# Kernel tuning notes

Hardware: AMD Instinct MI355X
Metric: run time of the kernel (lower is better)

Reference implementation:

```python
import jax, jax.numpy as jnp
import numpy as np

B, S, HID = 2, 2048, 1024
H, HKV, D = 16, 8, 128
G = H // HKV
EPS = 1e-6
ROPE_BASE = 1e6


def _rms_norm(x, w):
    # per-last-dim RMSNorm in fp32, matching QwenRMSNorm
    x32 = x.astype(jnp.float32)
    var = jnp.mean(x32 * x32, axis=-1, keepdims=True)
    return w * (x32 * jax.lax.rsqrt(var + EPS)).astype(x.dtype)


def _rotate_half(x):
    half = x.shape[-1] // 2
    return jnp.concatenate([-x[..., half:], x[..., :half]], axis=-1)


def setup_inputs() -> dict:
    key = jax.random.key(0)
    ks = jax.random.split(key, 6)
    return {
        "hidden_states": jax.random.normal(ks[0], (B, S, HID), dtype=jnp.float32),
        "position_ids": jnp.arange(S, dtype=jnp.int32),
        "Wq": jax.random.normal(ks[1], (HID, H * D), dtype=jnp.float32) * 0.02,
        "Wk": jax.random.normal(ks[2], (HID, HKV * D), dtype=jnp.float32) * 0.02,
        "Wv": jax.random.normal(ks[3], (HID, HKV * D), dtype=jnp.float32) * 0.02,
        "Wo": jax.random.normal(ks[4], (H * D, HID), dtype=jnp.float32) * 0.02,
        "q_norm_w": jnp.ones((D,), dtype=jnp.float32),
        "k_norm_w": jnp.ones((D,), dtype=jnp.float32),
    }


def reference(hidden_states, position_ids, Wq, Wk, Wv, Wo, q_norm_w, k_norm_w):
    b, s, _ = hidden_states.shape
    # projections
    q = (hidden_states @ Wq).reshape(b, s, H, D)
    k = (hidden_states @ Wk).reshape(b, s, HKV, D)
    v = (hidden_states @ Wv).reshape(b, s, HKV, D)
    # QK RMSNorm (per head_dim), then [B, heads, S, D]
    q = _rms_norm(q, q_norm_w).transpose(0, 2, 1, 3)
    k = _rms_norm(k, k_norm_w).transpose(0, 2, 1, 3)
    v = v.transpose(0, 2, 1, 3)
    # RoPE
    inv_freq = 1.0 / (ROPE_BASE ** (jnp.arange(0, D, 2, dtype=jnp.float32) / D))
    freqs = position_ids.astype(jnp.float32)[:, None] * inv_freq[None, :]  # [S, D/2]
    emb = jnp.concatenate([freqs, freqs], axis=-1)  # [S, D]
    cos = jnp.cos(emb)[None, None, :, :].astype(q.dtype)
    sin = jnp.sin(emb)[None, None, :, :].astype(q.dtype)
    q = q * cos + _rotate_half(q) * sin
    k = k * cos + _rotate_half(k) * sin
    # GQA attention without materializing repeated K/V:
    # q heads h = kh*G + g  <->  repeat_interleave(G, dim=1) of kv heads
    qg = q.reshape(b, HKV, G, s, D)
    scale = 1.0 / jnp.sqrt(jnp.asarray(D, dtype=q.dtype))
    scores = jnp.einsum('bhgqd,bhkd->bhgqk', qg, k) * scale  # [B,HKV,G,S,S]
    causal = jnp.tril(jnp.ones((s, s), dtype=bool))
    scores = jnp.where(causal[None, None, None, :, :], scores, jnp.finfo(scores.dtype).min)
    probs = jax.nn.softmax(scores, axis=-1)
    attn = jnp.einsum('bhgqk,bhkd->bhgqd', probs, v)  # [B,HKV,G,S,D]
    attn = attn.reshape(b, H, s, D).transpose(0, 2, 1, 3).reshape(b, s, H * D)
    out = attn @ Wo
    return out, k, v
```

## Files before the change

kernel.cpp:

```cpp
#include <hip/hip_runtime.h>

#define B_ 2
#define S_ 2048
#define HID_ 1024
#define H_ 16
#define HKV_ 8
#define D_ 128

typedef unsigned short u16;
typedef __attribute__((ext_vector_type(8))) short short8;
typedef __attribute__((ext_vector_type(4))) float f32x4;
typedef __attribute__((ext_vector_type(16))) float f32x16;
typedef __attribute__((ext_vector_type(2))) unsigned short u16x2;
typedef __attribute__((ext_vector_type(4))) unsigned short u16x4;
typedef const __attribute__((address_space(1))) void gvoid;
typedef __attribute__((address_space(3))) void svoid;

__device__ __forceinline__ u16 f2b(float f) {
  union { float f; unsigned u; } v; v.f = f;
  unsigned r = v.u + 0x7FFFu + ((v.u >> 16) & 1u);
  return (u16)(r >> 16);
}
__device__ __forceinline__ float b2f(u16 x) {
  union { unsigned u; float f; } v; v.u = ((unsigned)x) << 16; return v.f;
}

__device__ __forceinline__ float exp2_fast(float x) {
  float r; asm("v_exp_f32 %0, %1" : "=v"(r) : "v"(x)); return r;
}
__device__ __forceinline__ unsigned cvtpk_bf16(float lo, float hi) {
  unsigned r; asm("v_cvt_pk_bf16_f32 %0, %1, %2" : "=v"(r) : "v"(lo), "v"(hi)); return r;
}
__device__ __forceinline__ void vm_drain() {
  asm volatile("s_waitcnt vmcnt(0)" ::: "memory");
  __builtin_amdgcn_sched_barrier(0);
}

__global__ __launch_bounds__(256) void conv_bf16_kernel(const float* __restrict__ X,
                                                        u16* __restrict__ Y, int n4) {
  int i = blockIdx.x * 256 + threadIdx.x;
  if (i < n4) {
    const float4 v = ((const float4*)X)[i];
    u16x4 o = { f2b(v.x), f2b(v.y), f2b(v.z), f2b(v.w) };
    ((u16x4*)Y)[i] = o;
  }
}

template <bool PERM>
__global__ __launch_bounds__(256) void transpose_bf16_kernel(const float* __restrict__ W,
                                                             u16* __restrict__ Wt,
                                                             int K, int N) {
  __shared__ float t[32][33];
  const int nb = N >> 5;
  const int bx = blockIdx.x % nb;
  const int by = blockIdx.x / nb;
  const int tx = threadIdx.x & 31, ty = threadIdx.x >> 5;
#pragma unroll
  for (int i = 0; i < 32; i += 8)
    t[ty + i][tx] = W[(size_t)(by * 32 + ty + i) * N + bx * 32 + tx];
  __syncthreads();
#pragma unroll
  for (int i = 0; i < 32; i += 8) {
    int n = bx * 32 + ty + i;
    int nn;
    if (PERM) {
      int head = n >> 7, d = n & 127;
      int p = (d & 15) | (((d >> 6) & 1) << 4) | (((d >> 4) & 1) << 5) | (((d >> 5) & 1) << 6);
      nn = head * 128 + p;
    } else {
      nn = n;
    }
    Wt[(size_t)nn * K + by * 32 + tx] = f2b(t[tx][ty + i]);
  }
}

__global__ __launch_bounds__(256) void rope_table_kernel(const int* __restrict__ pid,
                                                         float* __restrict__ ct,
                                                         float* __restrict__ st) {
  int i = blockIdx.x * 256 + threadIdx.x;
  if (i >= 64 * S_) return;
  int f = i >> 11, s = i & 2047;
  double inv = exp2(-(double)f * (19.931568569324174 / 64.0));
  double ang = (double)pid[s] * inv;
  ct[i] = (float)cos(ang);
  st[i] = (float)sin(ang);
}

template <int M, int N, int K, int BM>
__global__ __launch_bounds__(256) void gemm_bt(const u16* __restrict__ A,
                                               const u16* __restrict__ Bt,
                                               float* __restrict__ C) {
  __shared__ u16 As[BM * 64];
  __shared__ u16 Bs[128 * 64];
  const int tid = threadIdx.x;
  const int w = tid >> 6;
  const int l = tid & 63;
  const int l15 = l & 15, lg = l >> 4;
  const int nbx = N / 128;
  const int bx = blockIdx.x % nbx, by = blockIdx.x / nbx;
  const int row0 = by * BM, col0 = bx * 128;
  const int wr = w >> 1, wc = w & 1;
  constexpr int MR = BM / 32;

  f32x4 acc[MR][4];
#pragma unroll
  for (int m = 0; m < MR; ++m)
#pragma unroll
    for (int n = 0; n < 4; ++n) acc[m][n] = (f32x4){0.f, 0.f, 0.f, 0.f};

  for (int k0 = 0; k0 < K; k0 += 64) {
    __syncthreads();
#pragma unroll
    for (int i = 0; i < BM / 32; ++i) {
      int c = i * 256 + tid;
      int r = c >> 3, cc = c & 7;
      int cs = cc ^ ((r ^ (r >> 3)) & 7);
      const u16* sa = A + (size_t)(row0 + r) * K + k0 + cs * 8;
      __builtin_amdgcn_global_load_lds((gvoid*)sa, (svoid*)(As + (i * 256 + w * 64) * 8), 16, 0, 0);
    }
#pragma unroll
    for (int i = 0; i < 4; ++i) {
      int c = i * 256 + tid;
      int r = c >> 3, cc = c & 7;
      int cs = cc ^ ((r ^ (r >> 3)) & 7);
      const u16* sb = Bt + (size_t)(col0 + r) * K + k0 + cs * 8;
      __builtin_amdgcn_global_load_lds((gvoid*)sb, (svoid*)(Bs + (i * 256 + w * 64) * 8), 16, 0, 0);
    }
    vm_drain();
    __syncthreads();
#pragma unroll
    for (int kk = 0; kk < 2; ++kk) {
      short8 af[MR], bf[4];
#pragma unroll
      for (int m = 0; m < MR; ++m) {
        const int row = wr * (BM / 2) + m * 16 + l15;
        af[m] = *(const short8*)((const char*)As + row * 128 +
                                 (((kk * 4 + lg) ^ ((row ^ (row >> 3)) & 7)) << 4));
      }
#pragma unroll
      for (int n = 0; n < 4; ++n) {
        const int row = wc * 64 + n * 16 + l15;
        bf[n] = *(const short8*)((const char*)Bs + row * 128 +
                                 (((kk * 4 + lg) ^ ((row ^ (row >> 3)) & 7)) << 4));
      }
#pragma unroll
      for (int m = 0; m < MR; ++m)
#pragma unroll
        for (int n = 0; n < 4; ++n)
          acc[m][n] = __builtin_amdgcn_mfma_f32_16x16x32_bf16(af[m], bf[n], acc[m][n], 0, 0, 0);
    }
  }
#pragma unroll
  for (int m = 0; m < MR; ++m)
#pragma unroll
    for (int n = 0; n < 4; ++n) {
      float* cp = C + (size_t)(row0 + wr * (BM / 2) + m * 16 + lg * 4) * N + col0 + wc * 64 + n * 16 + l15;
#pragma unroll
      for (int r = 0; r < 4; ++r) cp[(size_t)r * N] = acc[m][n][r];
    }
}

__global__ __launch_bounds__(256) void gemm_qkv_fused(const u16* __restrict__ A,
                                                      const u16* __restrict__ Bt,
                                                      const float* __restrict__ qnw,
                                                      const float* __restrict__ knw,
                                                      const float* __restrict__ ct_t,
                                                      const float* __restrict__ st_t,
                                                      u16* __restrict__ Qbb,
                                                      u16* __restrict__ Kbb,
                                                      float* __restrict__ kout,
                                                      float* __restrict__ vout,
                                                      u16* __restrict__ VTb) {
  constexpr int K = 1024;
  __shared__ u16 As[64 * 64];
  __shared__ u16 Bs[128 * 64];
  __shared__ float red[64][2];
  const int tid = threadIdx.x;
  const int w = tid >> 6;
  const int l = tid & 63;
  const int l15 = l & 15, lg = l >> 4;
  const int bx = blockIdx.x & 31, by = blockIdx.x >> 5;
  const int row0 = by * 64, col0 = bx * 128;
  const int wr = w >> 1, wc = w & 1;

  f32x4 acc[2][4];
#pragma unroll
  for (int m = 0; m < 2; ++m)
#pragma unroll
    for (int n = 0; n < 4; ++n) acc[m][n] = (f32x4){0.f, 0.f, 0.f, 0.f};

  for (int k0 = 0; k0 < K; k0 += 64) {
    __syncthreads();
#pragma unroll
    for (int i = 0; i < 2; ++i) {
      int c = i * 256 + tid;
      int r = c >> 3, cc = c & 7;
      int cs = cc ^ ((r ^ (r >> 3)) & 7);
      const u16* sa = A + (size_t)(row0 + r) * K + k0 + cs * 8;
      __builtin_amdgcn_global_load_lds((gvoid*)sa, (svoid*)(As + (i * 256 + w * 64) * 8), 16, 0, 0);
    }
#pragma unroll
    for (int i = 0; i < 4; ++i) {
      int c = i * 256 + tid;
      int r = c >> 3, cc = c & 7;
      int cs = cc ^ ((r ^ (r >> 3)) & 7);
      const u16* sb = Bt + (size_t)(col0 + r) * K + k0 + cs * 8;
      __builtin_amdgcn_global_load_lds((gvoid*)sb, (svoid*)(Bs + (i * 256 + w * 64) * 8), 16, 0, 0);
    }
    vm_drain();
    __syncthreads();
#pragma unroll
    for (int kk = 0; kk < 2; ++kk) {
      short8 af[2], bf[4];
#pragma unroll
      for (int m = 0; m < 2; ++m) {
        const int row = wr * 32 + m * 16 + l15;
        af[m] = *(const short8*)((const char*)As + row * 128 +
                                 (((kk * 4 + lg) ^ ((row ^ (row >> 3)) & 7)) << 4));
      }
#pragma unroll
      for (int n = 0; n < 4; ++n) {
        const int row = wc * 64 + n * 16 + l15;
        bf[n] = *(const short8*)((const char*)Bs + row * 128 +
                                 (((kk * 4 + lg) ^ ((row ^ (row >> 3)) & 7)) << 4));
      }
#pragma unroll
      for (int m = 0; m < 2; ++m)
#pragma unroll
        for (int n = 0; n < 4; ++n)
          acc[m][n] = __builtin_amdgcn_mfma_f32_16x16x32_bf16(af[m], bf[n], acc[m][n], 0, 0, 0);
    }
  }

  const int b_ = row0 >> 11;
  const int s0 = row0 & 2047;
  if (bx < 24) {
    float part[2][4];
#pragma unroll
    for (int m = 0; m < 2; ++m)
#pragma unroll
      for (int r = 0; r < 4; ++r) {
        float p = 0.f;
#pragma unroll
        for (int n = 0; n < 4; ++n) p += acc[m][n][r] * acc[m][n][r];
        part[m][r] = p;
      }
#pragma unroll
    for (int i = 1; i < 16; i <<= 1)
#pragma unroll
      for (int m = 0; m < 2; ++m)
#pragma unroll
        for (int r = 0; r < 4; ++r) part[m][r] += __shfl_xor(part[m][r], i, 64);
    if (l15 == 0) {
#pragma unroll
      for (int m = 0; m < 2; ++m)
#pragma unroll
        for (int r = 0; r < 4; ++r) red[wr * 32 + m * 16 + lg * 4 + r][wc] = part[m][r];
    }
    __syncthreads();

    const bool isQ = bx < 16;
    const int h = isQ ? bx : bx - 16;
    const float* nw = isQ ? qnw : knw;
    u16* outb = isQ ? Qbb : Kbb;
    const int NH = isQ ? 16 : 8;
#pragma unroll
    for (int np = 0; np < 2; ++np) {
      const int d_lo = l15 + 32 * wc + 16 * np;
      const float w_lo = nw[d_lo], w_hi = nw[d_lo + 64];
#pragma unroll
      for (int m = 0; m < 2; ++m) {
        const int sb = s0 + wr * 32 + m * 16 + lg * 4;
        const float4 cv = *(const float4*)(ct_t + d_lo * 2048 + sb);
        const float4 sv = *(const float4*)(st_t + d_lo * 2048 + sb);
#pragma unroll
        for (int r = 0; r < 4; ++r) {
          const int ro = wr * 32 + m * 16 + lg * 4 + r;
          const float tot = red[ro][0] + red[ro][1];
          const float rms = rsqrtf(tot * (1.0f / 128.0f) + 1e-6f);
          const float xl = acc[m][2 * np][r] * rms * w_lo;
          const float xh = acc[m][2 * np + 1][r] * rms * w_hi;
          const float cc = ((const float*)&cv)[r], ss = ((const float*)&sv)[r];
          const float ol = xl * cc - xh * ss;
          const float oh = xh * cc + xl * ss;
          const size_t base = ((size_t)(b_ * NH + h) * 2048 + sb + r) * 128;
          outb[base + d_lo] = f2b(ol);
          outb[base + d_lo + 64] = f2b(oh);
          if (!isQ) {
            kout[base + d_lo] = ol;
            kout[base + d_lo + 64] = oh;
          }
        }
      }
    }
  } else {
    const int h = bx - 24;
#pragma unroll
    for (int n = 0; n < 4; ++n) {
      const int d = wc * 64 + n * 16 + l15;
#pragma unroll
      for (int m = 0; m < 2; ++m) {
        const int sb = s0 + wr * 32 + m * 16 + lg * 4;
        u16x4 pk;
#pragma unroll
        for (int r = 0; r < 4; ++r) {
          const float x = acc[m][n][r];
          vout[((size_t)(b_ * 8 + h) * 2048 + sb + r) * 128 + d] = x;
          pk[r] = f2b(x);
        }
        *(u16x4*)(VTb + ((size_t)(b_ * 8 + h) * 128 + d) * 2048 + sb) = pk;
      }
    }
  }
}

__global__ __launch_bounds__(256, 2) void attn_kernel(const u16* __restrict__ Qb,
                                                      const u16* __restrict__ Kb,
                                                      const u16* __restrict__ VTb,
                                                      u16* __restrict__ Ab,
                                                      u16* __restrict__ Op,
                                                      float* __restrict__ Ml) {
  __shared__ u16 lds[2][16384];
  const int tid = threadIdx.x;
  const int w = tid >> 6, l = tid & 63;
  const int l31 = l & 31, hi = l >> 5;
  const int bid = blockIdx.x;
  const int half = bid & 1;
  const int pid = bid >> 1;
  const int b = pid >> 7;
  const int hh = (pid >> 3) & 15;
  const int p8 = pid & 7;
  const int hkv = hh >> 1;

  const u16* Kh = Kb + (size_t)(b * HKV_ + hkv) * S_ * 128;
  const u16* VTh = VTb + (size_t)(b * HKV_ + hkv) * 128 * S_;
  const float KSC = 0.12751740027f;
  int cur = 0;

  auto stage = [&](int kt, int buf) {
    const u16* Kp = Kh + (size_t)kt * 64 * 128;
    const u16* Vp = VTh + kt * 64;
    u16* Kd = &lds[buf][0];
    u16* Vd = &lds[buf][8192];
#pragma unroll
    for (int i = 0; i < 4; ++i) {
      int c = i * 256 + tid;
      int kr = c >> 4, kc = c & 15;
      int kcs = kc ^ ((kr ^ (kr >> 3)) & 15);
      __builtin_amdgcn_global_load_lds((gvoid*)(Kp + kr * 128 + kcs * 8),
                                       (svoid*)(Kd + (i * 256 + w * 64) * 8), 16, 0, 0);
      int vd = c >> 3, vc = c & 7;
      int vcs = vc ^ ((vd ^ (vd >> 3)) & 7);
      __builtin_amdgcn_global_load_lds((gvoid*)(Vp + (size_t)vd * S_ + vcs * 8),
                                       (svoid*)(Vd + (i * 256 + w * 64) * 8), 16, 0, 0);
    }
  };

  auto run_seg = [&](int pp, int kt0, int kt1, int mode) {
    const int q0 = pp * 128;
    const int ntp = 2 * (pp + 1);
    const int qrow = q0 + w * 32 + l31;

    short8 qf[8];
    {
      const u16* qp = Qb + ((size_t)(b * H_ + hh) * S_ + qrow) * 128 + hi * 8;
#pragma unroll
      for (int c = 0; c < 8; ++c) qf[c] = *(const short8*)(qp + c * 16);
    }

    float m_run = -1e30f, l_run = 0.f;
    f32x16 oacc[4];
#pragma unroll
    for (int n = 0; n < 4; ++n)
#pragma unroll
      for (int r = 0; r < 16; ++r) oacc[n][r] = 0.f;

    stage(kt0, cur);
    vm_drain();
    __syncthreads();
    for (int kt = kt0; kt < kt1; ++kt) {
      if (kt + 1 < kt1) stage(kt + 1, cur ^ 1);
      const u16* Kl = &lds[cur][0];
      const u16* Vl = &lds[cur][8192];
      const bool domask = (kt >= ntp - 2);

#pragma unroll
      for (int ts = 0; ts < 2; ++ts) {
        f32x16 stv0, stv1;
#pragma unroll
        for (int r = 0; r < 16; ++r) { stv0[r] = 0.f; stv1[r] = 0.f; }
        {
          const int row = ts * 32 + l31;
          const int rb = row * 256, sw = ((row ^ (row >> 3)) & 15) << 4;
          __builtin_amdgcn_s_setprio(1);
#pragma unroll
          for (int c = 0; c < 8; ++c) {
            short8 kf = *(const short8*)((const char*)Kl + rb + ((c * 32 + hi * 16) ^ sw));
            if (c & 1)
              stv1 = __builtin_amdgcn_mfma_f32_32x32x16_bf16(kf, qf[c], stv1, 0, 0, 0);
            else
              stv0 = __builtin_amdgcn_mfma_f32_32x32x16_bf16(kf, qf[c], stv0, 0, 0, 0);
          }
          __builtin_amdgcn_s_setprio(0);
        }

        float pvv[16];
        float mx = -1e30f;
#pragma unroll
        for (int r = 0; r < 16; ++r) {
          float x = (stv0[r] + stv1[r]) * KSC;
          if (domask) {
            int kv = kt * 64 + ts * 32 + (r & 3) + 8 * (r >> 2) + 4 * hi;
            if (kv > qrow) x = -1e30f;
          }
          pvv[r] = x;
          mx = fmaxf(mx, x);
        }
        mx = fmaxf(mx, __shfl_xor(mx, 32, 64));

        if (__any(mx > m_run + 8.0f)) {
          float mnew = fmaxf(m_run, mx);
          float corr = exp2_fast(m_run - mnew);
          l_run *= corr;
          m_run = mnew;
#pragma unroll
          for (int r = 0; r < 16; ++r) {
            float cr = __shfl(corr, (r & 3) + 8 * (r >> 2) + 4 * hi, 64);
#pragma unroll
            for (int n = 0; n < 4; ++n) oacc[n][r] *= cr;
          }
        }

        float ls = 0.f;
#pragma unroll
        for (int r = 0; r < 16; ++r) {
          float p = exp2_fast(pvv[r] - m_run);
          pvv[r] = p;
          ls += p;
        }
        l_run += ls + __shfl_xor(ls, 32, 64);

        unsigned W[4][2], Wx[4][2];
#pragma unroll
        for (int g = 0; g < 4; ++g)
#pragma unroll
          for (int i = 0; i < 2; ++i) {
            W[g][i] = cvtpk_bf16(pvv[4 * g + 2 * i], pvv[4 * g + 2 * i + 1]);
            Wx[g][i] = __shfl_xor(W[g][i], 32, 64);
          }

        __builtin_amdgcn_s_setprio(1);
#pragma unroll
        for (int cc = 0; cc < 2; ++cc) {
          short8 paf;
          ((unsigned*)&paf)[0] = hi ? Wx[2 * cc + 1][0] : W[2 * cc][0];
          ((unsigned*)&paf)[1] = hi ? Wx[2 * cc + 1][1] : W[2 * cc][1];
          ((unsigned*)&paf)[2] = hi ? W[2 * cc + 1][0] : Wx[2 * cc][0];
          ((unsigned*)&paf)[3] = hi ? W[2 * cc + 1][1] : Wx[2 * cc][1];
          const int cp = ts * 2 + cc;
#pragma unroll
          for (int n = 0; n < 4; ++n) {
            const int d = n * 32 + l31;
            const int swv = ((d ^ (d >> 3)) & 7) << 4;
            short8 vf = *(const short8*)((const char*)Vl + d * 128 + ((cp * 32 + hi * 16) ^ swv));
            oacc[n] = __builtin_amdgcn_mfma_f32_32x32x16_bf16(paf, vf, oacc[n], 0, 0, 0);
          }
        }
        __builtin_amdgcn_s_setprio(0);
      }
      vm_drain();
      __syncthreads();
      cur ^= 1;
    }

    if (mode == 0) {
#pragma unroll
      for (int r = 0; r < 16; ++r) {
        const int ql = (r & 3) + 8 * (r >> 2) + 4 * hi;
        float lb = __shfl(l_run, ql, 64);
        float inv = 1.0f / lb;
        const int q = q0 + w * 32 + ql;
        u16* op = Ab + ((size_t)(b * S_) + q) * 2048 + hh * 128 + l31;
#pragma unroll
        for (int n = 0; n < 4; ++n) op[n * 32] = f2b(oacc[n][r] * inv);
      }
    } else {
      const int part = mode - 1;
      u16* ob = Op + ((size_t)(part * 256 + pid)) * 128 * 128;
#pragma unroll
      for (int r = 0; r < 16; ++r) {
        const int ql = (r & 3) + 8 * (r >> 2) + 4 * hi;
        const int qq = w * 32 + ql;
#pragma unroll
        for (int n = 0; n < 4; ++n) ob[qq * 128 + n * 32 + l31] = f2b(oacc[n][r]);
      }
      if (hi == 0) {
        float* mlb = Ml + ((size_t)(part * 256 + pid)) * 256;
        mlb[w * 32 + l31] = m_run;
        mlb[128 + w * 32 + l31] = l_run;
      }
    }
  };

  if (half == 0) {
    run_seg(p8, 0, 2 * p8 + 2, 0);
    run_seg(15 - p8, 0, 15 - 2 * p8, 1);
  } else {
    run_seg(15 - p8, 15 - 2 * p8, 32 - 2 * p8, 2);
  }
}

__global__ __launch_bounds__(256) void attn_combine_kernel(const u16* __restrict__ Op,
                                                           const float* __restrict__ Ml,
                                                           u16* __restrict__ Ab) {
  const int pid = blockIdx.x;
  const int b = pid >> 7, hh = (pid >> 3) & 15, p8 = pid & 7;
  const int pp = 15 - p8;
  const int q = threadIdx.x >> 1;
  const int d0 = (threadIdx.x & 1) * 64;
  const float* ml0 = Ml + (size_t)pid * 256;
  const float* ml1 = Ml + (size_t)(256 + pid) * 256;
  const float m0 = ml0[q], l0 = ml0[128 + q];
  const float m1 = ml1[q], l1 = ml1[128 + q];
  const float m = fmaxf(m0, m1);
  const float w0 = exp2_fast(m0 - m), w1 = exp2_fast(m1 - m);
  const float linv = 1.0f / (w0 * l0 + w1 * l1);
  const u16* o0 = Op + ((size_t)pid * 128 + q) * 128 + d0;
  const u16* o1 = Op + ((size_t)(256 + pid) * 128 + q) * 128 + d0;
  u16* ab = Ab + ((size_t)(b * S_) + pp * 128 + q) * 2048 + hh * 128 + d0;
#pragma unroll
  for (int c = 0; c < 8; ++c) {
    short8 a = *(const short8*)(o0 + c * 8);
    short8 bb = *(const short8*)(o1 + c * 8);
    short8 o;
#pragma unroll
    for (int j = 0; j < 8; ++j)
      o[j] = (short)f2b((w0 * b2f((u16)a[j]) + w1 * b2f((u16)bb[j])) * linv);
    *(short8*)(ab + c * 8) = o;
  }
}

extern "C" void kernel_launch(void* const* d_in, const int* in_sizes, int n_in,
                              void* d_out, int out_size, void* d_ws, size_t ws_size,
                              hipStream_t stream) {
  const float* hs  = (const float*)d_in[0];
  const int*   pid = (const int*)d_in[1];
  const float* Wq  = (const float*)d_in[2];
  const float* Wk  = (const float*)d_in[3];
  const float* Wv  = (const float*)d_in[4];
  const float* Wo  = (const float*)d_in[5];
  const float* qnw = (const float*)d_in[6];
  const float* knw = (const float*)d_in[7];

  float* out0 = (float*)d_out;
  float* kout = out0 + (size_t)B_ * HKV_ * S_ * D_;
  float* vout = kout + (size_t)B_ * HKV_ * S_ * D_;

  char* ws = (char*)d_ws;
  size_t off = 0;
  auto alloc = [&](size_t bytes) {
    void* p = ws + off;
    off += (bytes + 255) & ~(size_t)255;
    return p;
  };
  u16*   Xb    = (u16*)alloc((size_t)4096 * 1024 * 2);
  u16*   Wqkvt = (u16*)alloc((size_t)4096 * 1024 * 2);
  u16*   Wot   = (u16*)alloc((size_t)1024 * 2048 * 2);
  float* ct_t  = (float*)alloc((size_t)64 * 2048 * 4);
  float* st_t  = (float*)alloc((size_t)64 * 2048 * 4);
  u16*   Qbb   = (u16*)alloc((size_t)B_ * H_ * S_ * D_ * 2);
  u16*   Kbb   = (u16*)alloc((size_t)B_ * HKV_ * S_ * D_ * 2);
  u16*   VTb   = (u16*)alloc((size_t)B_ * HKV_ * D_ * S_ * 2);
  u16*   Ab    = (u16*)alloc((size_t)B_ * S_ * H_ * D_ * 2);
  u16*   Op    = (u16*)alloc((size_t)2 * 256 * 128 * 128 * 2);
  float* Ml    = (float*)alloc((size_t)2 * 256 * 256 * 4);

  conv_bf16_kernel<<<4096, 256, 0, stream>>>(hs, Xb, 4096 * 1024 / 4);
  transpose_bf16_kernel<true><<<(2048 / 32) * (1024 / 32), 256, 0, stream>>>(Wq, Wqkvt, 1024, 2048);
  transpose_bf16_kernel<true><<<(1024 / 32) * (1024 / 32), 256, 0, stream>>>(Wk, Wqkvt + (size_t)2048 * 1024, 1024, 1024);
  transpose_bf16_kernel<false><<<(1024 / 32) * (1024 / 32), 256, 0, stream>>>(Wv, Wqkvt + (size_t)3072 * 1024, 1024, 1024);
  transpose_bf16_kernel<false><<<(1024 / 32) * (2048 / 32), 256, 0, stream>>>(Wo, Wot, 2048, 1024);
  rope_table_kernel<<<512, 256, 0, stream>>>(pid, ct_t, st_t);

  gemm_qkv_fused<<<2048, 256, 0, stream>>>(Xb, Wqkvt, qnw, knw, ct_t, st_t,
                                           Qbb, Kbb, kout, vout, VTb);

  attn_kernel<<<512, 256, 0, stream>>>(Qbb, Kbb, VTb, Ab, Op, Ml);
  attn_combine_kernel<<<256, 256, 0, stream>>>(Op, Ml, Ab);

  gemm_bt<4096, 1024, 2048, 64><<<8 * 64, 256, 0, stream>>>(Ab, Wot, out0);
}
```

Before: 172.7 us.

## Merge prep kernels into one launch, fold softmax scale into Q, tree-reduce max/sum

Six preprocessing launches (bf16 conversion of activations, the four weight transposes, and the RoPE table) become one prep kernel that dispatches on block index, which removes launch gaps. The softmax scale (1/sqrt(D)·log2e) is now applied to Q in the QKV epilogue, so the per-element multiply in the attention inner loop goes away. The QK MFMA now uses one accumulator instead of two alternating ones. Row max and sum become tree reductions to shorten dependency chains. The single accumulator puts back a serial MFMA dependency, and scaling Q before bf16 rounding changes numerics slightly.

After: 164.7 us. 4.6% less time.

```diff
diff --git a/kernel.cpp b/kernel.cpp
--- a/kernel.cpp
+++ b/kernel.cpp
@@ -36,24 +36,13 @@
   __builtin_amdgcn_sched_barrier(0);
 }
 
-__global__ __launch_bounds__(256) void conv_bf16_kernel(const float* __restrict__ X,
-                                                        u16* __restrict__ Y, int n4) {
-  int i = blockIdx.x * 256 + threadIdx.x;
-  if (i < n4) {
-    const float4 v = ((const float4*)X)[i];
-    u16x4 o = { f2b(v.x), f2b(v.y), f2b(v.z), f2b(v.w) };
-    ((u16x4*)Y)[i] = o;
-  }
-}
-
-template <bool PERM>
-__global__ __launch_bounds__(256) void transpose_bf16_kernel(const float* __restrict__ W,
-                                                             u16* __restrict__ Wt,
-                                                             int K, int N) {
-  __shared__ float t[32][33];
+__device__ __forceinline__ void transpose_dev(const float* __restrict__ W,
+                                              u16* __restrict__ Wt,
+                                              int K, int N, bool PERM, int bid,
+                                              float (*t)[33]) {
   const int nb = N >> 5;
-  const int bx = blockIdx.x % nb;
-  const int by = blockIdx.x / nb;
+  const int bx = bid % nb;
+  const int by = bid / nb;
   const int tx = threadIdx.x & 31, ty = threadIdx.x >> 5;
 #pragma unroll
   for (int i = 0; i < 32; i += 8)
@@ -74,16 +63,40 @@
   }
 }
 
-__global__ __launch_bounds__(256) void rope_table_kernel(const int* __restrict__ pid,
-                                                         float* __restrict__ ct,
-                                                         float* __restrict__ st) {
-  int i = blockIdx.x * 256 + threadIdx.x;
-  if (i >= 64 * S_) return;
-  int f = i >> 11, s = i & 2047;
-  double inv = exp2(-(double)f * (19.931568569324174 / 64.0));
-  double ang = (double)pid[s] * inv;
-  ct[i] = (float)cos(ang);
-  st[i] = (float)sin(ang);
+__global__ __launch_bounds__(256) void prep_kernel(const float* __restrict__ hs,
+                                                   u16* __restrict__ Xb,
+                                                   const float* __restrict__ Wq,
+                                                   const float* __restrict__ Wk,
+                                                   const float* __restrict__ Wv,
+                                                   const float* __restrict__ Wo,
+                                                   u16* __restrict__ Wqkvt,
+                                                   u16* __restrict__ Wot,
+                                                   const int* __restrict__ pid,
+                                                   float* __restrict__ ct,
+                                                   float* __restrict__ st) {
+  __shared__ float t[32][33];
+  const int bid = blockIdx.x;
+  if (bid < 4096) {
+    int i = bid * 256 + threadIdx.x;
+    const float4 v = ((const float4*)hs)[i];
+    u16x4 o = { f2b(v.x), f2b(v.y), f2b(v.z), f2b(v.w) };
+    ((u16x4*)Xb)[i] = o;
+  } else if (bid < 6144) {
+    transpose_dev(Wq, Wqkvt, 1024, 2048, true, bid - 4096, t);
+  } else if (bid < 7168) {
+    transpose_dev(Wk, Wqkvt + (size_t)2048 * 1024, 1024, 1024, true, bid - 6144, t);
+  } else if (bid < 8192) {
+    transpose_dev(Wv, Wqkvt + (size_t)3072 * 1024, 1024, 1024, false, bid - 7168, t);
+  } else if (bid < 10240) {
+    transpose_dev(Wo, Wot, 2048, 1024, false, bid - 8192, t);
+  } else {
+    int i = (bid - 10240) * 256 + threadIdx.x;
+    int f = i >> 11, s = i & 2047;
+    double inv = exp2(-(double)f * (19.931568569324174 / 64.0));
+    double ang = (double)pid[s] * inv;
+    ct[i] = (float)cos(ang);
+    st[i] = (float)sin(ang);
+  }
 }
 
 template <int M, int N, int K, int BM>
@@ -264,6 +277,7 @@
     const float* nw = isQ ? qnw : knw;
     u16* outb = isQ ? Qbb : Kbb;
     const int NH = isQ ? 16 : 8;
+    const float qsc = isQ ? 0.12751740027f : 1.0f;
 #pragma unroll
     for (int np = 0; np < 2; ++np) {
       const int d_lo = l15 + 32 * wc + 16 * np;
@@ -284,8 +298,8 @@
           const float ol = xl * cc - xh * ss;
           const float oh = xh * cc + xl * ss;
           const size_t base = ((size_t)(b_ * NH + h) * 2048 + sb + r) * 128;
-          outb[base + d_lo] = f2b(ol);
-          outb[base + d_lo + 64] = f2b(oh);
+          outb[base + d_lo] = f2b(ol * qsc);
+          outb[base + d_lo + 64] = f2b(oh * qsc);
           if (!isQ) {
             kout[base + d_lo] = ol;
             kout[base + d_lo + 64] = oh;
@@ -334,7 +348,6 @@
 
   const u16* Kh = Kb + (size_t)(b * HKV_ + hkv) * S_ * 128;
   const u16* VTh = VTb + (size_t)(b * HKV_ + hkv) * 128 * S_;
-  const float KSC = 0.12751740027f;
   int cur = 0;
 
   auto stage = [&](int kt, int buf) {
@@ -386,9 +399,9 @@
 
 #pragma unroll
       for (int ts = 0; ts < 2; ++ts) {
-        f32x16 stv0, stv1;
-#pragma unroll
-        for (int r = 0; r < 16; ++r) { stv0[r] = 0.f; stv1[r] = 0.f; }
+        f32x16 stv;
+#pragma unroll
+        for (int r = 0; r < 16; ++r) stv[r] = 0.f;
         {
           const int row = ts * 32 + l31;
           const int rb = row * 256, sw = ((row ^ (row >> 3)) & 15) << 4;
@@ -396,26 +409,27 @@
 #pragma unroll
           for (int c = 0; c < 8; ++c) {
             short8 kf = *(const short8*)((const char*)Kl + rb + ((c * 32 + hi * 16) ^ sw));
-            if (c & 1)
-              stv1 = __builtin_amdgcn_mfma_f32_32x32x16_bf16(kf, qf[c], stv1, 0, 0, 0);
-            else
-              stv0 = __builtin_amdgcn_mfma_f32_32x32x16_bf16(kf, qf[c], stv0, 0, 0, 0);
+            stv = __builtin_amdgcn_mfma_f32_32x32x16_bf16(kf, qf[c], stv, 0, 0, 0);
           }
           __builtin_amdgcn_s_setprio(0);
         }
 
         float pvv[16];
-        float mx = -1e30f;
 #pragma unroll
         for (int r = 0; r < 16; ++r) {
-          float x = (stv0[r] + stv1[r]) * KSC;
+          float x = stv[r];
           if (domask) {
             int kv = kt * 64 + ts * 32 + (r & 3) + 8 * (r >> 2) + 4 * hi;
             if (kv > qrow) x = -1e30f;
           }
           pvv[r] = x;
-          mx = fmaxf(mx, x);
         }
+        float t0[8];
+#pragma unroll
+        for (int r = 0; r < 8; ++r) t0[r] = fmaxf(pvv[r], pvv[r + 8]);
+#pragma unroll
+        for (int r = 0; r < 4; ++r) t0[r] = fmaxf(t0[r], t0[r + 4]);
+        float mx = fmaxf(fmaxf(t0[0], t0[1]), fmaxf(t0[2], t0[3]));
         mx = fmaxf(mx, __shfl_xor(mx, 32, 64));
 
         if (__any(mx > m_run + 8.0f)) {
@@ -431,13 +445,14 @@
           }
         }
 
-        float ls = 0.f;
-#pragma unroll
-        for (int r = 0; r < 16; ++r) {
-          float p = exp2_fast(pvv[r] - m_run);
-          pvv[r] = p;
-          ls += p;
-        }
+#pragma unroll
+        for (int r = 0; r < 16; ++r) pvv[r] = exp2_fast(pvv[r] - m_run);
+        float s0[8];
+#pragma unroll
+        for (int r = 0; r < 8; ++r) s0[r] = pvv[r] + pvv[r + 8];
+#pragma unroll
+        for (int r = 0; r < 4; ++r) s0[r] = s0[r] + s0[r + 4];
+        float ls = (s0[0] + s0[1]) + (s0[2] + s0[3]);
         l_run += ls + __shfl_xor(ls, 32, 64);
 
         unsigned W[4][2], Wx[4][2];
@@ -575,12 +590,8 @@
   u16*   Op    = (u16*)alloc((size_t)2 * 256 * 128 * 128 * 2);
   float* Ml    = (float*)alloc((size_t)2 * 256 * 256 * 4);
 
-  conv_bf16_kernel<<<4096, 256, 0, stream>>>(hs, Xb, 4096 * 1024 / 4);
-  transpose_bf16_kernel<true><<<(2048 / 32) * (1024 / 32), 256, 0, stream>>>(Wq, Wqkvt, 1024, 2048);
-  transpose_bf16_kernel<true><<<(1024 / 32) * (1024 / 32), 256, 0, stream>>>(Wk, Wqkvt + (size_t)2048 * 1024, 1024, 1024);
-  transpose_bf16_kernel<false><<<(1024 / 32) * (1024 / 32), 256, 0, stream>>>(Wv, Wqkvt + (size_t)3072 * 1024, 1024, 1024);
-  transpose_bf16_kernel<false><<<(1024 / 32) * (2048 / 32), 256, 0, stream>>>(Wo, Wot, 2048, 1024);
-  rope_table_kernel<<<512, 256, 0, stream>>>(pid, ct_t, st_t);
+  prep_kernel<<<10752, 256, 0, stream>>>(hs, Xb, Wq, Wk, Wv, Wo, Wqkvt, Wot,
+                                         pid, ct_t, st_t);
 
   gemm_qkv_fused<<<2048, 256, 0, stream>>>(Xb, Wqkvt, qnw, knw, ct_t, st_t,
                                            Qbb, Kbb, kout, vout, VTb);
```
